# Optimization experiments

Measured on AMD Instinct MI355X. Metric: run time of the kernel, lower is better.

Reference implementation:

```python
import jax, jax.numpy as jnp
import numpy as np

N_NODES = 50000
N_EDGES = 400000
D_IN, D_HID, D_OUT = 512, 512, 256


def setup_inputs() -> dict:
    key = jax.random.key(0)
    k = jax.random.split(key, 6)
    x = jax.random.normal(k[0], (N_NODES, D_IN), dtype=jnp.float32)
    edge_index = jax.random.randint(k[1], (2, N_EDGES), 0, N_NODES, dtype=jnp.int64)
    # Glorot-ish init for the two GCNConv linear layers
    W1 = jax.random.normal(k[2], (D_IN, D_HID), dtype=jnp.float32) * (1.0 / np.sqrt(D_IN))
    b1 = jnp.zeros((D_HID,), dtype=jnp.float32)
    W2 = jax.random.normal(k[3], (D_HID, D_OUT), dtype=jnp.float32) * (1.0 / np.sqrt(D_HID))
    b2 = jnp.zeros((D_OUT,), dtype=jnp.float32)
    return {"x": x, "edge_index": edge_index, "W1": W1, "b1": b1, "W2": W2, "b2": b2}


def _gcn_conv(x, W, b, src, dst, norm, n):
    """PyG GCNConv: h = x W; out[i] = sum_{j->i} norm_e * h[j] + b.
    src/dst already include self-loops; norm = d^-1/2[src] * d^-1/2[dst]."""
    h = x @ W  # [n, d_out]
    msgs = h[src] * norm[:, None]  # gather + scale per edge
    agg = jnp.zeros((n, h.shape[1]), dtype=h.dtype).at[dst].add(msgs)  # scatter-add
    return agg + b


def reference(x, edge_index, W1, b1, W2, b2):
    n = x.shape[0]
    loop = jnp.arange(n, dtype=edge_index.dtype)
    src = jnp.concatenate([edge_index[0], loop])  # add self-loops
    dst = jnp.concatenate([edge_index[1], loop])
    # symmetric normalization on the self-loop-augmented graph
    deg = jnp.zeros((n,), dtype=x.dtype).at[dst].add(1.0)
    dinv = jnp.where(deg > 0, jax.lax.rsqrt(deg), 0.0)
    norm = dinv[src] * dinv[dst]
    h = jax.nn.relu(_gcn_conv(x, W1, b1, src, dst, norm, n))
    return _gcn_conv(h, W2, b2, src, dst, norm, n)
```

## Files before the change

kernel.cpp:

```cpp
#include <hip/hip_runtime.h>
#include <stdint.h>

typedef __bf16 bf16_t;
typedef __bf16 bf16x8 __attribute__((ext_vector_type(8)));
typedef float f32x4 __attribute__((ext_vector_type(4)));
typedef uint32_t u32x4 __attribute__((ext_vector_type(4)));

#define N_NODES  50000
#define N_EDGES  400000
#define D_IN     512
#define D_HID    512
#define D_OUTD   256
#define M_PAD    50048
#define NB_SCAN  196

__device__ __forceinline__ uint32_t f2bf_bits(float x){
    uint32_t u = __float_as_uint(x);
    return (u + 0x7fffu + ((u >> 16) & 1u)) >> 16;
}
__device__ __forceinline__ void unpack8(uint4 v, float* f){
    f[0]=__uint_as_float(v.x<<16); f[1]=__uint_as_float(v.x & 0xffff0000u);
    f[2]=__uint_as_float(v.y<<16); f[3]=__uint_as_float(v.y & 0xffff0000u);
    f[4]=__uint_as_float(v.z<<16); f[5]=__uint_as_float(v.z & 0xffff0000u);
    f[6]=__uint_as_float(v.w<<16); f[7]=__uint_as_float(v.w & 0xffff0000u);
}
__device__ __forceinline__ void glds16(const bf16_t* g, bf16_t* l){
    __builtin_amdgcn_global_load_lds(
        (const __attribute__((address_space(1))) uint32_t*)g,
        (__attribute__((address_space(3))) uint32_t*)l, 16, 0, 0);
}

__global__ __launch_bounds__(256)
void conv_x_bf16(const float* __restrict__ x, bf16_t* __restrict__ Xb,
                 int* __restrict__ deg){
    const int t = blockIdx.x * 256 + threadIdx.x;
    if (t < N_NODES) deg[t] = 1;
    const int row = t >> 7;
    uint2 o;
    if (row < N_NODES){
        f32x4 v = __builtin_nontemporal_load(((const f32x4*)x) + t);
        o.x = f2bf_bits(v.x) | (f2bf_bits(v.y) << 16);
        o.y = f2bf_bits(v.z) | (f2bf_bits(v.w) << 16);
    } else { o.x = 0u; o.y = 0u; }
    ((uint2*)Xb)[t] = o;
}

__global__ __launch_bounds__(256)
void conv_w_both(const float* __restrict__ W1, const float* __restrict__ W2,
                 bf16_t* __restrict__ W1t, bf16_t* __restrict__ W2t,
                 const int* __restrict__ ei, int* __restrict__ deg){
    const int idx = blockIdx.x * 256 + threadIdx.x;
    if (idx < N_EDGES) atomicAdd(&deg[ei[N_EDGES + idx]], 1);
    const int n = idx >> 9;
    const int k = idx & 511;
    if (n < 512) W1t[idx] = (bf16_t)W1[k * 512 + n];
    else if (n < 768) W2t[(n - 512) * 512 + k] = (bf16_t)W2[k * 256 + (n - 512)];
}

__global__ __launch_bounds__(256)
void k_scan_dinv(const int* __restrict__ deg, float* __restrict__ dinv,
                 int* __restrict__ part, int* __restrict__ bsum, int n){
    __shared__ int tmp[256];
    int i = blockIdx.x*256 + threadIdx.x;
    int d = (i < n) ? deg[i] : 1;
    if (i < n) dinv[i] = rsqrtf((float)d);
    int v = (i < n) ? (d - 1) : 0;
    tmp[threadIdx.x] = v;
    __syncthreads();
    for (int off = 1; off < 256; off <<= 1){
        int t = (threadIdx.x >= off) ? tmp[threadIdx.x - off] : 0;
        __syncthreads();
        tmp[threadIdx.x] += t;
        __syncthreads();
    }
    if (i < n) part[i] = tmp[threadIdx.x] - v;
    if (threadIdx.x == 255) bsum[blockIdx.x] = tmp[255];
}
__global__ __launch_bounds__(256)
void k_scan_bsum(const int* __restrict__ bsum, int* __restrict__ bsum2, int nb){
    __shared__ int tmp[256];
    int v = (threadIdx.x < nb) ? bsum[threadIdx.x] : 0;
    tmp[threadIdx.x] = v;
    __syncthreads();
    for (int off = 1; off < 256; off <<= 1){
        int t = (threadIdx.x >= off) ? tmp[threadIdx.x - off] : 0;
        __syncthreads();
        tmp[threadIdx.x] += t;
        __syncthreads();
    }
    if (threadIdx.x < nb) bsum2[threadIdx.x] = tmp[threadIdx.x] - v;
}
__global__ __launch_bounds__(256)
void k_finalize_rowptr(const int* __restrict__ part, const int* __restrict__ bsum2,
                       int* __restrict__ rowp, int* __restrict__ cursor, int n){
    int i = blockIdx.x*256 + threadIdx.x;
    if (i < n){ int r = part[i] + bsum2[blockIdx.x]; rowp[i] = r; cursor[i] = r; }
    if (i == 0) rowp[n] = N_EDGES;
}
__global__ __launch_bounds__(256)
void k_place(const int* __restrict__ ei, const float* __restrict__ dinv,
             int* __restrict__ cursor, int* __restrict__ csrc, float* __restrict__ cnorm){
    int e = blockIdx.x*256 + threadIdx.x;
    if (e < N_EDGES){
        int s = ei[e];
        int d = ei[N_EDGES + e];
        int p = atomicAdd(&cursor[d], 1);
        csrc[p]  = s;
        cnorm[p] = dinv[s] * dinv[d];
    }
}

__global__ __launch_bounds__(256, 2)
void gemm_bf16_mfma(const bf16_t* __restrict__ A, const bf16_t* __restrict__ Bt,
                    bf16_t* __restrict__ C, int N, int K)
{
    __shared__ bf16_t As[128*32];
    __shared__ bf16_t Bs[256*32];

    const int tid  = threadIdx.x;
    const int lane = tid & 63;
    const int wave = tid >> 6;
    const int wr = wave >> 1;
    const int wc = wave & 1;
    const int mBase = blockIdx.x * 128;
    const int nBase = blockIdx.y * 256;

    const int srow = tid >> 2;
    const int scol = (tid & 3) << 3;
    const bf16_t* Ag0 = A  + (size_t)(mBase + srow) * K + scol;
    const bf16_t* Ag1 = A  + (size_t)(mBase + 64 + srow) * K + scol;
    const bf16_t* Bg[4];
    #pragma unroll
    for (int c = 0; c < 4; ++c)
        Bg[c] = Bt + (size_t)(nBase + c*64 + srow) * K + scol;

    const int m16 = lane & 15;
    const int q   = lane >> 4;
    const bf16_t* aP = &As[(wr*64 + m16)*32 + q*8];
    const bf16_t* bP = &Bs[(wc*128 + m16)*32 + q*8];

    f32x4 acc[4][8] = {};

    for (int k0 = 0; k0 < K; k0 += 32){
        glds16(Ag0 + k0, &As[(size_t)tid * 8]);
        glds16(Ag1 + k0, &As[(size_t)(256 + tid) * 8]);
        #pragma unroll
        for (int c = 0; c < 4; ++c)
            glds16(Bg[c] + k0, &Bs[(size_t)(c*256 + tid) * 8]);
        __syncthreads();
        bf16x8 a[4], b[8];
        #pragma unroll
        for (int t = 0; t < 4; ++t) a[t] = *(const bf16x8*)(aP + t*16*32);
        #pragma unroll
        for (int t = 0; t < 8; ++t) b[t] = *(const bf16x8*)(bP + t*16*32);
        #pragma unroll
        for (int i = 0; i < 4; ++i){
            #pragma unroll
            for (int j = 0; j < 8; ++j){
                acc[i][j] = __builtin_amdgcn_mfma_f32_16x16x32_bf16(a[i], b[j], acc[i][j], 0, 0, 0);
            }
        }
        __syncthreads();
    }

    #pragma unroll
    for (int i = 0; i < 4; ++i){
        const int row0 = mBase + wr*64 + i*16 + q*4;
        #pragma unroll
        for (int j = 0; j < 8; ++j){
            const int col = nBase + wc*128 + j*16 + m16;
            bf16_t* Cp = C + (size_t)row0 * N + col;
            #pragma unroll
            for (int r = 0; r < 4; ++r)
                Cp[(size_t)r * N] = (bf16_t)acc[i][j][r];
        }
    }
}

__global__ __launch_bounds__(256)
void agg_bias_relu_512(const bf16_t* __restrict__ T, const int* __restrict__ rowp,
                       const int* __restrict__ csrc, const float* __restrict__ cnorm,
                       const float* __restrict__ dinv, const float* __restrict__ bias,
                       bf16_t* __restrict__ H)
{
    const int gw   = (blockIdx.x * 256 + threadIdx.x) >> 6;
    const int lane = threadIdx.x & 63;
    if (gw >= N_NODES) return;
    const float di = dinv[gw];
    const uint4* Tr = (const uint4*)T;
    float acc[8];
    {
        uint4 v = Tr[(size_t)gw * 64 + lane];
        float f[8]; unpack8(v, f);
        const float w = di * di;
        #pragma unroll
        for (int j = 0; j < 8; ++j) acc[j] = w * f[j];
    }
    int e = rowp[gw];
    const int e1 = rowp[gw + 1];

    if (e + 4 <= e1){
        uint4 v0, v1, v2, v3; float w0, w1, w2, w3;
        {
            const int s0 = csrc[e], s1 = csrc[e+1], s2 = csrc[e+2], s3 = csrc[e+3];
            w0 = cnorm[e]; w1 = cnorm[e+1]; w2 = cnorm[e+2]; w3 = cnorm[e+3];
            v0 = Tr[(size_t)s0 * 64 + lane];
            v1 = Tr[(size_t)s1 * 64 + lane];
            v2 = Tr[(size_t)s2 * 64 + lane];
            v3 = Tr[(size_t)s3 * 64 + lane];
        }
        e += 4;
        for (; e + 4 <= e1; e += 4){
            const int   t0 = csrc[e],   t1 = csrc[e+1], t2 = csrc[e+2], t3 = csrc[e+3];
            const float x0 = cnorm[e],  x1 = cnorm[e+1], x2 = cnorm[e+2], x3 = cnorm[e+3];
            uint4 n0 = Tr[(size_t)t0 * 64 + lane];
            uint4 n1 = Tr[(size_t)t1 * 64 + lane];
            uint4 n2 = Tr[(size_t)t2 * 64 + lane];
            uint4 n3 = Tr[(size_t)t3 * 64 + lane];
            float f[8];
            unpack8(v0, f);
            #pragma unroll
            for (int j = 0; j < 8; ++j) acc[j] += w0 * f[j];
            unpack8(v1, f);
            #pragma unroll
            for (int j = 0; j < 8; ++j) acc[j] += w1 * f[j];
            unpack8(v2, f);
            #pragma unroll
            for (int j = 0; j < 8; ++j) acc[j] += w2 * f[j];
            unpack8(v3, f);
            #pragma unroll
            for (int j = 0; j < 8; ++j) acc[j] += w3 * f[j];
            v0 = n0; v1 = n1; v2 = n2; v3 = n3;
            w0 = x0; w1 = x1; w2 = x2; w3 = x3;
        }
        float f[8];
        unpack8(v0, f);
        #pragma unroll
        for (int j = 0; j < 8; ++j) acc[j] += w0 * f[j];
        unpack8(v1, f);
        #pragma unroll
        for (int j = 0; j < 8; ++j) acc[j] += w1 * f[j];
        unpack8(v2, f);
        #pragma unroll
        for (int j = 0; j < 8; ++j) acc[j] += w2 * f[j];
        unpack8(v3, f);
        #pragma unroll
        for (int j = 0; j < 8; ++j) acc[j] += w3 * f[j];
    }
    for (; e < e1; ++e){
        const int   s = csrc[e];
        const float w = cnorm[e];
        uint4 v = Tr[(size_t)s * 64 + lane];
        float f[8]; unpack8(v, f);
        #pragma unroll
        for (int j = 0; j < 8; ++j) acc[j] += w * f[j];
    }
    const float4 b0 = ((const float4*)bias)[lane*2];
    const float4 b1 = ((const float4*)bias)[lane*2 + 1];
    float r[8] = {acc[0]+b0.x, acc[1]+b0.y, acc[2]+b0.z, acc[3]+b0.w,
                  acc[4]+b1.x, acc[5]+b1.y, acc[6]+b1.z, acc[7]+b1.w};
    u32x4 o;
    o.x = f2bf_bits(fmaxf(r[0],0.f)) | (f2bf_bits(fmaxf(r[1],0.f)) << 16);
    o.y = f2bf_bits(fmaxf(r[2],0.f)) | (f2bf_bits(fmaxf(r[3],0.f)) << 16);
    o.z = f2bf_bits(fmaxf(r[4],0.f)) | (f2bf_bits(fmaxf(r[5],0.f)) << 16);
    o.w = f2bf_bits(fmaxf(r[6],0.f)) | (f2bf_bits(fmaxf(r[7],0.f)) << 16);
    __builtin_nontemporal_store(o, ((u32x4*)(H + (size_t)gw * 512)) + lane);
}

__global__ __launch_bounds__(256)
void agg_bias_out_256(const bf16_t* __restrict__ T, const int* __restrict__ rowp,
                      const int* __restrict__ csrc, const float* __restrict__ cnorm,
                      const float* __restrict__ dinv, const float* __restrict__ bias,
                      float* __restrict__ out)
{
    const int wid  = (blockIdx.x * 256 + threadIdx.x) >> 6;
    const int half = (threadIdx.x >> 5) & 1;
    const int l32  = threadIdx.x & 31;
    const int node = wid * 2 + half;
    if (node >= N_NODES) return;
    const float di = dinv[node];
    float acc[8];
    {
        uint4 v = ((const uint4*)(T + (size_t)node * 256))[l32];
        float f[8]; unpack8(v, f);
        const float w = di * di;
        #pragma unroll
        for (int j = 0; j < 8; ++j) acc[j] = w * f[j];
    }
    int e = rowp[node];
    const int e1 = rowp[node + 1];
    for (; e + 4 <= e1; e += 4){
        const int   s0 = csrc[e],   s1 = csrc[e+1], s2 = csrc[e+2], s3 = csrc[e+3];
        const float w0 = cnorm[e],  w1 = cnorm[e+1], w2 = cnorm[e+2], w3 = cnorm[e+3];
        uint4 v0 = ((const uint4*)(T + (size_t)s0 * 256))[l32];
        uint4 v1 = ((const uint4*)(T + (size_t)s1 * 256))[l32];
        uint4 v2 = ((const uint4*)(T + (size_t)s2 * 256))[l32];
        uint4 v3 = ((const uint4*)(T + (size_t)s3 * 256))[l32];
        float f[8];
        unpack8(v0, f);
        #pragma unroll
        for (int j = 0; j < 8; ++j) acc[j] += w0 * f[j];
        unpack8(v1, f);
        #pragma unroll
        for (int j = 0; j < 8; ++j) acc[j] += w1 * f[j];
        unpack8(v2, f);
        #pragma unroll
        for (int j = 0; j < 8; ++j) acc[j] += w2 * f[j];
        unpack8(v3, f);
        #pragma unroll
        for (int j = 0; j < 8; ++j) acc[j] += w3 * f[j];
    }
    for (; e < e1; ++e){
        const int   s = csrc[e];
        const float w = cnorm[e];
        uint4 v = ((const uint4*)(T + (size_t)s * 256))[l32];
        float f[8]; unpack8(v, f);
        #pragma unroll
        for (int j = 0; j < 8; ++j) acc[j] += w * f[j];
    }
    const float4 b0 = ((const float4*)bias)[l32*2];
    const float4 b1 = ((const float4*)bias)[l32*2 + 1];
    f32x4 o0 = {acc[0]+b0.x, acc[1]+b0.y, acc[2]+b0.z, acc[3]+b0.w};
    f32x4 o1 = {acc[4]+b1.x, acc[5]+b1.y, acc[6]+b1.z, acc[7]+b1.w};
    __builtin_nontemporal_store(o0, ((f32x4*)(out + (size_t)node * 256)) + l32*2);
    __builtin_nontemporal_store(o1, ((f32x4*)(out + (size_t)node * 256)) + l32*2 + 1);
}

extern "C" void kernel_launch(void* const* d_in, const int* in_sizes, int n_in,
                              void* d_out, int out_size, void* d_ws, size_t ws_size,
                              hipStream_t stream)
{
    const float* x  = (const float*)d_in[0];
    const int*   ei = (const int*)d_in[1];
    const float* W1 = (const float*)d_in[2];
    const float* b1 = (const float*)d_in[3];
    const float* W2 = (const float*)d_in[4];
    const float* b2 = (const float*)d_in[5];
    float* out = (float*)d_out;

    char* w = (char*)d_ws;
    auto alloc = [&](size_t bytes) -> char* {
        char* p = w; w += (bytes + 255) & ~(size_t)255; return p;
    };
    bf16_t* Xb    = (bf16_t*)alloc((size_t)M_PAD * 512 * 2);
    bf16_t* T     = (bf16_t*)alloc((size_t)M_PAD * 512 * 2);
    bf16_t* W1t   = (bf16_t*)alloc(512 * 512 * 2);
    bf16_t* W2t   = (bf16_t*)alloc(256 * 512 * 2);
    int*    deg   = (int*)  alloc(N_NODES * 4);
    float*  dinv  = (float*)alloc(N_NODES * 4);
    int*    rowp  = (int*)  alloc((N_NODES + 1) * 4);
    int*    cursor= (int*)  alloc(N_NODES * 4);
    int*    part  = (int*)  alloc(N_NODES * 4);
    int*    bsum  = (int*)  alloc(NB_SCAN * 4);
    int*    bsum2 = (int*)  alloc(NB_SCAN * 4);
    int*    csrc  = (int*)  alloc(N_EDGES * 4);
    float*  cnorm = (float*)alloc(N_EDGES * 4);

    conv_x_bf16<<<(M_PAD*128)/256, 256, 0, stream>>>(x, Xb, deg);
    conv_w_both<<<1568, 256, 0, stream>>>(W1, W2, W1t, W2t, ei, deg);

    k_scan_dinv<<<NB_SCAN, 256, 0, stream>>>(deg, dinv, part, bsum, N_NODES);
    k_scan_bsum <<<1, 256, 0, stream>>>(bsum, bsum2, NB_SCAN);
    k_finalize_rowptr<<<NB_SCAN, 256, 0, stream>>>(part, bsum2, rowp, cursor, N_NODES);
    k_place   <<<(N_EDGES+255)/256, 256, 0, stream>>>(ei, dinv, cursor, csrc, cnorm);

    gemm_bf16_mfma<<<dim3(M_PAD/128, 512/256), 256, 0, stream>>>(Xb, W1t, T, 512, 512);
    agg_bias_relu_512<<<(N_NODES+3)/4, 256, 0, stream>>>(T, rowp, csrc, cnorm, dinv, b1, Xb);

    gemm_bf16_mfma<<<dim3(M_PAD/128, 256/256), 256, 0, stream>>>(Xb, W2t, T, 256, 512);
    agg_bias_out_256<<<(25000+3)/4, 256, 0, stream>>>(T, rowp, csrc, cnorm, dinv, b2, out);
}
```

Before: 392.5 us.

## Fuse fp32-to-bf16 conversion of x into first GEMM A-tile load

Drops the separate pass that converts x to a bf16 buffer. The first GEMM now reads fp32 x directly, converts it in registers and writes it to LDS. The new GEMM uses a 128x512 tile with 512 threads, so each block covers the full output width and reads x only once. This removes an extra write and read of a 50 MB intermediate, but the A-tile load is now synchronous global-to-register with no prefetch, and the larger accumulator tile raises register pressure.

```diff
diff --git a/kernel.cpp b/kernel.cpp
--- a/kernel.cpp
+++ b/kernel.cpp
@@ -31,18 +31,9 @@
 }
 
 __global__ __launch_bounds__(256)
-void conv_x_bf16(const float* __restrict__ x, bf16_t* __restrict__ Xb,
-                 int* __restrict__ deg){
-    const int t = blockIdx.x * 256 + threadIdx.x;
-    if (t < N_NODES) deg[t] = 1;
-    const int row = t >> 7;
-    uint2 o;
-    if (row < N_NODES){
-        f32x4 v = __builtin_nontemporal_load(((const f32x4*)x) + t);
-        o.x = f2bf_bits(v.x) | (f2bf_bits(v.y) << 16);
-        o.y = f2bf_bits(v.z) | (f2bf_bits(v.w) << 16);
-    } else { o.x = 0u; o.y = 0u; }
-    ((uint2*)Xb)[t] = o;
+void k_init_deg(int* __restrict__ deg){
+    int i = blockIdx.x*256 + threadIdx.x;
+    if (i < N_NODES) deg[i] = 1;
 }
 
 __global__ __launch_bounds__(256)
@@ -107,6 +98,81 @@
         int p = atomicAdd(&cursor[d], 1);
         csrc[p]  = s;
         cnorm[p] = dinv[s] * dinv[d];
+    }
+}
+
+__global__ __launch_bounds__(512)
+void gemm1_fused(const float* __restrict__ x, const bf16_t* __restrict__ W1t,
+                 bf16_t* __restrict__ T)
+{
+    __shared__ bf16_t As[128*32];
+    __shared__ bf16_t Bs[512*32];
+
+    const int tid  = threadIdx.x;
+    const int lane = tid & 63;
+    const int wave = tid >> 6;
+    const int wr = wave >> 2;
+    const int wc = wave & 3;
+    const int mBase = blockIdx.x * 128;
+
+    const int arow = tid >> 2;
+    const int acol = (tid & 3) << 3;
+    const bool avalid = (mBase + arow) < N_NODES;
+    const float* Ag = x + (size_t)(mBase + arow) * 512 + acol;
+
+    const bf16_t* Bg[4];
+    #pragma unroll
+    for (int c = 0; c < 4; ++c)
+        Bg[c] = W1t + (size_t)(c*128 + arow) * 512 + acol;
+
+    const int m16 = lane & 15;
+    const int q   = lane >> 4;
+    const bf16_t* aP = &As[(wr*64 + m16)*32 + q*8];
+    const bf16_t* bP = &Bs[(wc*128 + m16)*32 + q*8];
+
+    f32x4 acc[4][8] = {};
+
+    for (int k0 = 0; k0 < 512; k0 += 32){
+        #pragma unroll
+        for (int c = 0; c < 4; ++c)
+            glds16(Bg[c] + k0, &Bs[(size_t)(c*512 + tid) * 8]);
+        uint4 aw = {0u, 0u, 0u, 0u};
+        if (avalid){
+            f32x4 v0 = __builtin_nontemporal_load((const f32x4*)(Ag + k0));
+            f32x4 v1 = __builtin_nontemporal_load((const f32x4*)(Ag + k0 + 4));
+            aw.x = f2bf_bits(v0.x) | (f2bf_bits(v0.y) << 16);
+            aw.y = f2bf_bits(v0.z) | (f2bf_bits(v0.w) << 16);
+            aw.z = f2bf_bits(v1.x) | (f2bf_bits(v1.y) << 16);
+            aw.w = f2bf_bits(v1.z) | (f2bf_bits(v1.w) << 16);
+        }
+        *(uint4*)(&As[arow*32 + acol]) = aw;
+        __syncthreads();
+        bf16x8 a[4], b[8];
+        #pragma unroll
+        for (int t = 0; t < 4; ++t) a[t] = *(const bf16x8*)(aP + t*16*32);
+        #pragma unroll
+        for (int t = 0; t < 8; ++t) b[t] = *(const bf16x8*)(bP + t*16*32);
+        #pragma unroll
+        for (int i = 0; i < 4; ++i){
+            #pragma unroll
+            for (int j = 0; j < 8; ++j){
+                acc[i][j] = __builtin_amdgcn_mfma_f32_16x16x32_bf16(a[i], b[j], acc[i][j], 0, 0, 0);
+            }
+        }
+        __syncthreads();
+    }
+
+    #pragma unroll
+    for (int i = 0; i < 4; ++i){
+        const int row0 = mBase + wr*64 + i*16 + q*4;
+        #pragma unroll
+        for (int j = 0; j < 8; ++j){
+            const int col = wc*128 + j*16 + m16;
+            bf16_t* Cp = T + (size_t)row0 * 512 + col;
+            #pragma unroll
+            for (int r = 0; r < 4; ++r)
+                Cp[(size_t)r * 512] = (bf16_t)acc[i][j][r];
+        }
     }
 }
 
@@ -342,7 +408,7 @@
     auto alloc = [&](size_t bytes) -> char* {
         char* p = w; w += (bytes + 255) & ~(size_t)255; return p;
     };
-    bf16_t* Xb    = (bf16_t*)alloc((size_t)M_PAD * 512 * 2);
+    bf16_t* Hb    = (bf16_t*)alloc((size_t)M_PAD * 512 * 2);
     bf16_t* T     = (bf16_t*)alloc((size_t)M_PAD * 512 * 2);
     bf16_t* W1t   = (bf16_t*)alloc(512 * 512 * 2);
     bf16_t* W2t   = (bf16_t*)alloc(256 * 512 * 2);
@@ -356,7 +422,7 @@
     int*    csrc  = (int*)  alloc(N_EDGES * 4);
     float*  cnorm = (float*)alloc(N_EDGES * 4);
 
-    conv_x_bf16<<<(M_PAD*128)/256, 256, 0, stream>>>(x, Xb, deg);
+    k_init_deg<<<NB_SCAN, 256, 0, stream>>>(deg);
     conv_w_both<<<1568, 256, 0, stream>>>(W1, W2, W1t, W2t, ei, deg);
 
     k_scan_dinv<<<NB_SCAN, 256, 0, stream>>>(deg, dinv, part, bsum, N_NODES);
@@ -364,9 +430,9 @@
     k_finalize_rowptr<<<NB_SCAN, 256, 0, stream>>>(part, bsum2, rowp, cursor, N_NODES);
     k_place   <<<(N_EDGES+255)/256, 256, 0, stream>>>(ei, dinv, cursor, csrc, cnorm);
 
-    gemm_bf16_mfma<<<dim3(M_PAD/128, 512/256), 256, 0, stream>>>(Xb, W1t, T, 512, 512);
-    agg_bias_relu_512<<<(N_NODES+3)/4, 256, 0, stream>>>(T, rowp, csrc, cnorm, dinv, b1, Xb);
-
-    gemm_bf16_mfma<<<dim3(M_PAD/128, 256/256), 256, 0, stream>>>(Xb, W2t, T, 256, 512);
+    gemm1_fused<<<M_PAD/128, 512, 0, stream>>>(x, W1t, T);
+    agg_bias_relu_512<<<(N_NODES+3)/4, 256, 0, stream>>>(T, rowp, csrc, cnorm, dinv, b1, Hb);
+
+    gemm_bf16_mfma<<<dim3(M_PAD/128, 256/256), 256, 0, stream>>>(Hb, W2t, T, 256, 512);
     agg_bias_out_256<<<(25000+3)/4, 256, 0, stream>>>(T, rowp, csrc, cnorm, dinv, b2, out);
 }
```

New measurement: 398.2 us. About the same (+1.4%).
